# Kernel optimization log

Measured on AMD Instinct MI355X. Metric: run time of the kernel, lower is better.

## Reference

```python
import jax, jax.numpy as jnp
import numpy as np

D_MODEL = 512
NHEAD = 8
DIM = D_MODEL // NHEAD
EPS_ATT = 1e-6
EPS_LN = 1e-5


def layer_norm(x, gamma, beta):
    mu = jnp.mean(x, axis=-1, keepdims=True)
    var = jnp.mean(jnp.square(x - mu), axis=-1, keepdims=True)
    return (x - mu) * jax.lax.rsqrt(var + EPS_LN) * gamma + beta


def setup_inputs() -> dict:
    key = jax.random.key(0)
    ks = jax.random.split(key, 12)
    B, L = 4, 4096
    s = 1.0 / np.sqrt(D_MODEL)
    inp = {
        "q": jax.random.normal(ks[0], (B, L, D_MODEL), jnp.float32),
        "k": jax.random.normal(ks[1], (B, L, D_MODEL), jnp.float32),
        "v": jax.random.normal(ks[2], (B, L, D_MODEL), jnp.float32),
        # weights stored [in, out] so application is x @ W (== torch Linear with W.T)
        "Wq": jax.random.normal(ks[3], (D_MODEL, D_MODEL), jnp.float32) * s,
        "Wk": jax.random.normal(ks[4], (D_MODEL, D_MODEL), jnp.float32) * s,
        "Wv": jax.random.normal(ks[5], (D_MODEL, D_MODEL), jnp.float32) * s,
        "Wm": jax.random.normal(ks[6], (D_MODEL, D_MODEL), jnp.float32) * s,
        "W1": jax.random.normal(ks[7], (D_MODEL, 4 * D_MODEL), jnp.float32) * s,
        "W2": jax.random.normal(ks[8], (4 * D_MODEL, D_MODEL), jnp.float32) * (0.5 * s),
        "g1": jnp.ones((D_MODEL,), jnp.float32),
        "b1": jnp.zeros((D_MODEL,), jnp.float32),
        "g2": jnp.ones((D_MODEL,), jnp.float32),
        "b2": jnp.zeros((D_MODEL,), jnp.float32),
    }
    return inp


def reference(q, k, v, Wq, Wk, Wv, Wm, W1, W2, g1, b1, g2, b2):
    B, L, _ = q.shape
    S = k.shape[1]
    # projections -> [B, L, H, D]
    Qp = (q @ Wq).reshape(B, L, NHEAD, DIM)
    Kp = (k @ Wk).reshape(B, S, NHEAD, DIM)
    Vp = (v @ Wv).reshape(B, S, NHEAD, DIM)
    # elu+1 feature map linear attention
    Q = jax.nn.elu(Qp) + 1.0
    K = jax.nn.elu(Kp) + 1.0
    Vn = Vp / S
    KV = jnp.einsum('nshd,nshv->nhdv', K, Vn)          # [B,H,D,D]
    Z = 1.0 / (jnp.einsum('nlhd,nhd->nlh', Q, K.sum(axis=1)) + EPS_ATT)
    msg = jnp.einsum('nlhd,nhdv,nlh->nlhv', Q, KV, Z) * S  # [B,L,H,D]
    # merge + residual + norm1
    msg = msg.reshape(B, L, D_MODEL) @ Wm
    msg = layer_norm(msg + q, g1, b1)
    # FFN; note original adds mlp output to q (not norm1 output)
    ffn = jax.nn.relu(msg @ W1) @ W2
    out = layer_norm(q + ffn, g2, b2)
    return out
```

## Files before the change

kernel.cpp:

```cpp
#include <hip/hip_runtime.h>

typedef unsigned short u16;
typedef unsigned int u32;

typedef __bf16 bf16x8 __attribute__((ext_vector_type(8)));
typedef float f32x4 __attribute__((ext_vector_type(4)));

#define EPI_BF16 0
#define EPI_ELU1 1
#define EPI_RELU 2
#define EPI_ADDRES_F32 3

__device__ __forceinline__ float bf2f(u16 x) {
    u32 u = ((u32)x) << 16;
    return __uint_as_float(u);
}
__device__ __forceinline__ u16 f2bf(float f) {
    u32 u = __float_as_uint(f);
    u32 r = (u + 0x7FFFu + ((u >> 16) & 1u)) >> 16;
    return (u16)r;
}

__device__ __forceinline__ void gload_lds16(const u16* g, u16* l) {
    __builtin_amdgcn_global_load_lds(
        (const __attribute__((address_space(1))) u32*)g,
        (__attribute__((address_space(3))) u32*)l, 16, 0, 0);
}

__global__ __launch_bounds__(256) void f2b_k(const float* __restrict__ in,
                                             u16* __restrict__ out, int n) {
    int i = (blockIdx.x * 256 + threadIdx.x) * 4;
    if (i >= n) return;
    float4 f = *(const float4*)(in + i);
    ushort4 o;
    o.x = f2bf(f.x); o.y = f2bf(f.y); o.z = f2bf(f.z); o.w = f2bf(f.w);
    *(ushort4*)(out + i) = o;
}

__global__ void transpose_k(const float* __restrict__ in, u16* __restrict__ out,
                            int R, int C) {
    int idx = blockIdx.x * 256 + threadIdx.x;
    if (idx >= R * C) return;
    int c = idx / R, r = idx % R;
    out[idx] = f2bf(in[(long)r * C + c]);
}

__global__ __launch_bounds__(256) void gemm_bt(
    const u16* __restrict__ A, const u16* __restrict__ Bt,
    void* __restrict__ C, const float* __restrict__ Res,
    int M, int N, int K, int epi)
{
    __shared__ __align__(16) u16 As[2][128 * 32];
    __shared__ __align__(16) u16 Bs[2][128 * 32];

    int t = threadIdx.x;

    int gx = gridDim.x;
    int nwg = gx * gridDim.y;
    int bid = blockIdx.y * gx + blockIdx.x;
    if ((nwg & 7) == 0) {
        int cpx = nwg >> 3;
        bid = (bid & 7) * cpx + (bid >> 3);
    }
    int m0 = (bid / gx) * 128, n0 = (bid % gx) * 128;

    int wave = t >> 6, lane = t & 63;
    int wm = (wave >> 1) * 64, wn = (wave & 1) * 64;
    int lrow = lane & 15, lk8 = (lane >> 4) * 8;

    f32x4 acc[4][4] = {};

    int srow = wave * 16 + (lane >> 2);
    int scol = (lane & 3) * 8;
    const u16* pA0 = A + (long)(m0 + srow) * K + scol;
    const u16* pB0 = Bt + (long)(n0 + srow) * K + scol;
    const long s64 = (long)64 * K;

    int nt = K >> 5;
    int cur = 0;

    {
        u16* a = As[0] + wave * 512;
        u16* b = Bs[0] + wave * 512;
        gload_lds16(pA0, a);
        gload_lds16(pA0 + s64, a + 2048);
        gload_lds16(pB0, b);
        gload_lds16(pB0 + s64, b + 2048);
    }
    __builtin_amdgcn_s_waitcnt(0);
    __syncthreads();

    for (int kt = 0; kt < nt; ++kt) {
        if (kt + 1 < nt) {
            int k0 = (kt + 1) << 5;
            u16* a = As[cur ^ 1] + wave * 512;
            u16* b = Bs[cur ^ 1] + wave * 512;
            gload_lds16(pA0 + k0, a);
            gload_lds16(pA0 + s64 + k0, a + 2048);
            gload_lds16(pB0 + k0, b);
            gload_lds16(pB0 + s64 + k0, b + 2048);
        }

        const u16* As_c = As[cur];
        const u16* Bs_c = Bs[cur];
        bf16x8 af[4], bfr[4];
#pragma unroll
        for (int mi = 0; mi < 4; mi++)
            af[mi] = *(const bf16x8*)(As_c + (wm + mi * 16 + lrow) * 32 + lk8);
#pragma unroll
        for (int ni = 0; ni < 4; ni++)
            bfr[ni] = *(const bf16x8*)(Bs_c + (wn + ni * 16 + lrow) * 32 + lk8);
#pragma unroll
        for (int mi = 0; mi < 4; mi++)
#pragma unroll
            for (int ni = 0; ni < 4; ni++)
                acc[mi][ni] = __builtin_amdgcn_mfma_f32_16x16x32_bf16(
                    af[mi], bfr[ni], acc[mi][ni], 0, 0, 0);

        if (kt + 1 < nt) {
            __builtin_amdgcn_s_waitcnt(0);
            __syncthreads();
            cur ^= 1;
        }
    }

    int rq = (lane >> 4) * 4;
    int colb = n0 + wn + (lane & 15);
#pragma unroll
    for (int mi = 0; mi < 4; mi++) {
#pragma unroll
        for (int ni = 0; ni < 4; ni++) {
#pragma unroll
            for (int r = 0; r < 4; r++) {
                int row = m0 + wm + mi * 16 + rq + r;
                int col = colb + ni * 16;
                long idx = (long)row * N + col;
                float v0 = acc[mi][ni][r];
                if (epi == EPI_ELU1) {
                    float v = v0 > 0.f ? v0 + 1.f : __expf(v0);
                    ((u16*)C)[idx] = f2bf(v);
                } else if (epi == EPI_RELU) {
                    ((u16*)C)[idx] = f2bf(v0 > 0.f ? v0 : 0.f);
                } else if (epi == EPI_ADDRES_F32) {
                    ((float*)C)[idx] = v0 + Res[idx];
                } else {
                    ((u16*)C)[idx] = f2bf(v0);
                }
            }
        }
    }
}

__global__ __launch_bounds__(256) void kv_part(
    const u16* __restrict__ Kf, const u16* __restrict__ Vf,
    float* __restrict__ Part, float* __restrict__ KsPart)
{
    __shared__ float sKf[64 * 68];
    __shared__ float sVf[64 * 68];
    int bh = blockIdx.x;
    int b = bh >> 3, h = bh & 7;
    int s0 = blockIdx.y * 64;
    int t = threadIdx.x;
    int d = t & 63, vg = t >> 6;

    {
        int row = t >> 2, c16 = (t & 3) * 16;
        long g = ((long)b * 4096 + s0 + row) * 512 + h * 64 + c16;
        uint4 kk0 = *(const uint4*)(Kf + g);
        uint4 kk1 = *(const uint4*)(Kf + g + 8);
        uint4 vv0 = *(const uint4*)(Vf + g);
        uint4 vv1 = *(const uint4*)(Vf + g + 8);
        float* dk = sKf + row * 68 + c16;
        float* dv = sVf + row * 68 + c16;
        u32 kw[8] = {kk0.x, kk0.y, kk0.z, kk0.w, kk1.x, kk1.y, kk1.z, kk1.w};
        u32 vw[8] = {vv0.x, vv0.y, vv0.z, vv0.w, vv1.x, vv1.y, vv1.z, vv1.w};
#pragma unroll
        for (int j = 0; j < 8; j++) {
            dk[2 * j]     = __uint_as_float(kw[j] << 16);
            dk[2 * j + 1] = __uint_as_float(kw[j] & 0xFFFF0000u);
            dv[2 * j]     = __uint_as_float(vw[j] << 16);
            dv[2 * j + 1] = __uint_as_float(vw[j] & 0xFFFF0000u);
        }
    }
    __syncthreads();

    float acc[16] = {};
    float ks = 0.f;
#pragma unroll 4
    for (int s = 0; s < 64; s++) {
        float kd = sKf[s * 68 + d];
        if (vg == 0) ks += kd;
        const float* vr = sVf + s * 68 + vg * 16;
        float4 v0 = *(const float4*)(vr);
        float4 v1 = *(const float4*)(vr + 4);
        float4 v2 = *(const float4*)(vr + 8);
        float4 v3 = *(const float4*)(vr + 12);
        acc[0]  += kd * v0.x; acc[1]  += kd * v0.y;
        acc[2]  += kd * v0.z; acc[3]  += kd * v0.w;
        acc[4]  += kd * v1.x; acc[5]  += kd * v1.y;
        acc[6]  += kd * v1.z; acc[7]  += kd * v1.w;
        acc[8]  += kd * v2.x; acc[9]  += kd * v2.y;
        acc[10] += kd * v2.z; acc[11] += kd * v2.w;
        acc[12] += kd * v3.x; acc[13] += kd * v3.y;
        acc[14] += kd * v3.z; acc[15] += kd * v3.w;
    }
    float* pp = Part + ((long)bh * 64 + blockIdx.y) * 4096 + d * 64 + vg * 16;
#pragma unroll
    for (int j = 0; j < 16; j++) pp[j] = acc[j];
    if (vg == 0) KsPart[((bh * 64) + blockIdx.y) * 64 + d] = ks;
}

__global__ __launch_bounds__(256) void kv_reduce(
    const float* __restrict__ Part, const float* __restrict__ KsPart,
    float* __restrict__ KV, float* __restrict__ Ksum)
{
    int i = blockIdx.x * 256 + threadIdx.x;
    if (i < 131072) {
        int bh = i >> 12, dv = i & 4095;
        const float* p = Part + (long)bh * 64 * 4096 + dv;
        float s = 0.f;
#pragma unroll 8
        for (int sp = 0; sp < 64; sp++) s += p[(long)sp * 4096];
        KV[i] = s;
    } else if (i < 133120) {
        int j = i - 131072;
        int bh = j >> 6, d = j & 63;
        const float* p = KsPart + bh * 64 * 64 + d;
        float s = 0.f;
#pragma unroll 8
        for (int sp = 0; sp < 64; sp++) s += p[sp * 64];
        Ksum[j] = s;
    }
}

__global__ __launch_bounds__(256) void msg_k(
    const u16* __restrict__ Q, const float* __restrict__ KV,
    const float* __restrict__ Ksum, u16* __restrict__ Msg)
{
    __shared__ float sKVt[64 * 68];
    __shared__ float sQ[64 * 68];
    __shared__ float sKs[64];
    __shared__ float sZ[64];

    int bh = blockIdx.x;
    int b = bh >> 3, h = bh & 7;
    int l0 = blockIdx.y * 64;
    int t = threadIdx.x, wave = t >> 6, lane = t & 63;

    {
        const float* src = KV + (long)bh * 4096 + t * 16;
        int d = t >> 2;
        int v0 = (t & 3) * 16;
        float4 a0 = *(const float4*)(src);
        float4 a1 = *(const float4*)(src + 4);
        float4 a2 = *(const float4*)(src + 8);
        float4 a3 = *(const float4*)(src + 12);
        float tmp[16] = {a0.x, a0.y, a0.z, a0.w, a1.x, a1.y, a1.z, a1.w,
                         a2.x, a2.y, a2.z, a2.w, a3.x, a3.y, a3.z, a3.w};
#pragma unroll
        for (int j = 0; j < 16; j++) sKVt[(v0 + j) * 68 + d] = tmp[j];
    }
    {
        int row = t >> 2, c = (t & 3) * 16;
        const u16* src = Q + ((long)b * 4096 + l0 + row) * 512 + h * 64 + c;
        uint4 q0 = *(const uint4*)(src);
        uint4 q1 = *(const uint4*)(src + 8);
        float* dq = sQ + row * 68 + c;
        u32 qw[8] = {q0.x, q0.y, q0.z, q0.w, q1.x, q1.y, q1.z, q1.w};
#pragma unroll
        for (int j = 0; j < 8; j++) {
            dq[2 * j]     = __uint_as_float(qw[j] << 16);
            dq[2 * j + 1] = __uint_as_float(qw[j] & 0xFFFF0000u);
        }
    }
    if (t < 64) sKs[t] = Ksum[bh * 64 + t];
    __syncthreads();

    float kv[64];
    {
        const float* kr = sKVt + lane * 68;
#pragma unroll
        for (int j = 0; j < 16; j++) {
            float4 x = *(const float4*)(kr + 4 * j);
            kv[4 * j]     = x.x; kv[4 * j + 1] = x.y;
            kv[4 * j + 2] = x.z; kv[4 * j + 3] = x.w;
        }
    }
    if (t < 64) {
        const float* qr = sQ + t * 68;
        float zp = 0.f;
#pragma unroll
        for (int d = 0; d < 64; d++) zp += qr[d] * sKs[d];
        sZ[t] = 1.f / (zp + 1e-6f);
    }
    __syncthreads();

    const long obase = ((long)b * 4096 + l0) * 512 + h * 64 + lane;
    int lbase = wave * 16;
#pragma unroll 4
    for (int i = 0; i < 16; i++) {
        int ll = lbase + i;
        const float* qr = sQ + ll * 68;
        float a0 = 0.f, a1 = 0.f, a2 = 0.f, a3 = 0.f;
#pragma unroll
        for (int db = 0; db < 16; db++) {
            float4 q4 = *(const float4*)(qr + 4 * db);
            a0 += q4.x * kv[4 * db];
            a1 += q4.y * kv[4 * db + 1];
            a2 += q4.z * kv[4 * db + 2];
            a3 += q4.w * kv[4 * db + 3];
        }
        float acc = (a0 + a1) + (a2 + a3);
        Msg[obase + (long)ll * 512] = f2bf(acc * sZ[ll]);
    }
}

__global__ __launch_bounds__(256) void ln_k(
    const float* __restrict__ X, const float* __restrict__ g,
    const float* __restrict__ bta, u16* __restrict__ OutB,
    float* __restrict__ OutF, int out_f32)
{
    int row = blockIdx.x;
    const float* x = X + (long)row * 512;
    int t = threadIdx.x;
    float x0 = x[t], x1 = x[t + 256];
    float s = x0 + x1, sq = x0 * x0 + x1 * x1;
#pragma unroll
    for (int off = 32; off > 0; off >>= 1) {
        s += __shfl_xor(s, off, 64);
        sq += __shfl_xor(sq, off, 64);
    }
    __shared__ float rs[4], rq[4];
    int wave = t >> 6, lane = t & 63;
    if (lane == 0) { rs[wave] = s; rq[wave] = sq; }
    __syncthreads();
    s = rs[0] + rs[1] + rs[2] + rs[3];
    sq = rq[0] + rq[1] + rq[2] + rq[3];
    float mu = s * (1.f / 512.f);
    float var = sq * (1.f / 512.f) - mu * mu;
    float rstd = rsqrtf(var + 1e-5f);
    float y0 = (x0 - mu) * rstd * g[t] + bta[t];
    float y1 = (x1 - mu) * rstd * g[t + 256] + bta[t + 256];
    if (out_f32) {
        OutF[(long)row * 512 + t] = y0;
        OutF[(long)row * 512 + t + 256] = y1;
    } else {
        OutB[(long)row * 512 + t] = f2bf(y0);
        OutB[(long)row * 512 + t + 256] = f2bf(y1);
    }
}

extern "C" void kernel_launch(void* const* d_in, const int* in_sizes, int n_in,
                              void* d_out, int out_size, void* d_ws, size_t ws_size,
                              hipStream_t stream) {
    const float* q  = (const float*)d_in[0];
    const float* k  = (const float*)d_in[1];
    const float* v  = (const float*)d_in[2];
    const float* Wq = (const float*)d_in[3];
    const float* Wk = (const float*)d_in[4];
    const float* Wv = (const float*)d_in[5];
    const float* Wm = (const float*)d_in[6];
    const float* W1 = (const float*)d_in[7];
    const float* W2 = (const float*)d_in[8];
    const float* g1 = (const float*)d_in[9];
    const float* b1 = (const float*)d_in[10];
    const float* g2 = (const float*)d_in[11];
    const float* b2 = (const float*)d_in[12];

    char* ws = (char*)d_ws;
    u16* WTq = (u16*)(ws + 0);
    u16* WTk = (u16*)(ws + 524288);
    u16* WTv = (u16*)(ws + 1048576);
    u16* WTm = (u16*)(ws + 1572864);
    u16* W1T = (u16*)(ws + 2097152);
    u16* W2T = (u16*)(ws + 4194304);
    u16* qc  = (u16*)(ws + 6291456);
    u16* kc  = (u16*)(ws + 23068672);
    u16* vc  = (u16*)(ws + 39845888);
    u16* Qb  = (u16*)(ws + 56623104);
    u16* Kb  = (u16*)(ws + 73400320);
    u16* Vb  = (u16*)(ws + 90177536);
    float* KVb = (float*)(ws + 106954752);
    float* KSb = (float*)(ws + 107479040);
    u16* Msg = (u16*)(ws + 107487232);
    float* Part = (float*)(ws + 23068672);
    float* KsPart = (float*)(ws + 6291456);
    float* xpre = (float*)(ws + 23068672);
    u16* x1  = qc;
    u16* Hid = (u16*)(ws + 56623104);

    f2b_k<<<dim3(8192), 256, 0, stream>>>(q, qc, 8388608);
    f2b_k<<<dim3(8192), 256, 0, stream>>>(k, kc, 8388608);
    f2b_k<<<dim3(8192), 256, 0, stream>>>(v, vc, 8388608);

    transpose_k<<<dim3(1024), 256, 0, stream>>>(Wq, WTq, 512, 512);
    transpose_k<<<dim3(1024), 256, 0, stream>>>(Wk, WTk, 512, 512);
    transpose_k<<<dim3(1024), 256, 0, stream>>>(Wv, WTv, 512, 512);
    transpose_k<<<dim3(1024), 256, 0, stream>>>(Wm, WTm, 512, 512);
    transpose_k<<<dim3(4096), 256, 0, stream>>>(W1, W1T, 512, 2048);
    transpose_k<<<dim3(4096), 256, 0, stream>>>(W2, W2T, 2048, 512);

    gemm_bt<<<dim3(4, 128), 256, 0, stream>>>(qc, WTq, Qb, nullptr, 16384, 512, 512, EPI_ELU1);
    gemm_bt<<<dim3(4, 128), 256, 0, stream>>>(kc, WTk, Kb, nullptr, 16384, 512, 512, EPI_ELU1);
    gemm_bt<<<dim3(4, 128), 256, 0, stream>>>(vc, WTv, Vb, nullptr, 16384, 512, 512, EPI_BF16);

    kv_part<<<dim3(32, 64), 256, 0, stream>>>(Kb, Vb, Part, KsPart);
    kv_reduce<<<dim3(520), 256, 0, stream>>>(Part, KsPart, KVb, KSb);
    msg_k<<<dim3(32, 64), 256, 0, stream>>>(Qb, KVb, KSb, Msg);

    gemm_bt<<<dim3(4, 128), 256, 0, stream>>>(Msg, WTm, xpre, q, 16384, 512, 512, EPI_ADDRES_F32);
    ln_k<<<dim3(16384), 256, 0, stream>>>(xpre, g1, b1, x1, nullptr, 0);

    gemm_bt<<<dim3(16, 128), 256, 0, stream>>>(x1, W1T, Hid, nullptr, 16384, 2048, 512, EPI_RELU);
    gemm_bt<<<dim3(4, 128), 256, 0, stream>>>(Hid, W2T, xpre, q, 16384, 512, 2048, EPI_ADDRES_F32);
    ln_k<<<dim3(16384), 256, 0, stream>>>(xpre, g2, b2, nullptr, (float*)d_out, 1);
}
```

Measured before the change: 519.9 us.

## Deepen GEMM LDS pipeline to four stages with k-group-major LDS layout

Replaces the double-buffered LDS pipeline in the bf16 GEMM with a 4-buffer ring that prefetches three k-tiles ahead. It uses partial vmcnt waits so outstanding global->LDS loads can overlap compute instead of draining every iteration. It also changes the staging layout so each lane loads one row's 8-element k-group and LDS is stored k-group-major, making MFMA fragment reads contiguous and likely reducing bank conflicts. LDS usage doubles to 64KB per block, which may reduce occupancy. Correctness now depends on the hand-counted vmcnt values.

```diff
diff --git a/kernel.cpp b/kernel.cpp
--- a/kernel.cpp
+++ b/kernel.cpp
@@ -50,8 +50,8 @@
     void* __restrict__ C, const float* __restrict__ Res,
     int M, int N, int K, int epi)
 {
-    __shared__ __align__(16) u16 As[2][128 * 32];
-    __shared__ __align__(16) u16 Bs[2][128 * 32];
+    __shared__ __align__(16) u16 As[4][4096];
+    __shared__ __align__(16) u16 Bs[4][4096];
 
     int t = threadIdx.x;
 
@@ -66,62 +66,61 @@
 
     int wave = t >> 6, lane = t & 63;
     int wm = (wave >> 1) * 64, wn = (wave & 1) * 64;
-    int lrow = lane & 15, lk8 = (lane >> 4) * 8;
+    int lrow = lane & 15;
+    int lg = lane >> 4;
 
     f32x4 acc[4][4] = {};
 
-    int srow = wave * 16 + (lane >> 2);
-    int scol = (lane & 3) * 8;
-    const u16* pA0 = A + (long)(m0 + srow) * K + scol;
-    const u16* pB0 = Bt + (long)(n0 + srow) * K + scol;
-    const long s64 = (long)64 * K;
+    int srow = (wave & 1) * 64 + lane;
+    int sg8 = (wave >> 1) * 8;
+    const u16* pA0 = A + (long)(m0 + srow) * K + sg8;
+    const u16* pB0 = Bt + (long)(n0 + srow) * K + sg8;
 
     int nt = K >> 5;
-    int cur = 0;
-
-    {
-        u16* a = As[0] + wave * 512;
-        u16* b = Bs[0] + wave * 512;
-        gload_lds16(pA0, a);
-        gload_lds16(pA0 + s64, a + 2048);
-        gload_lds16(pB0, b);
-        gload_lds16(pB0 + s64, b + 2048);
-    }
-    __builtin_amdgcn_s_waitcnt(0);
-    __syncthreads();
+
+    for (int pt = 0; pt < 3 && pt < nt; ++pt) {
+        int k0 = pt << 5;
+        u16* a = As[pt] + wave * 512;
+        u16* b = Bs[pt] + wave * 512;
+        gload_lds16(pA0 + k0, a);
+        gload_lds16(pA0 + k0 + 16, a + 2048);
+        gload_lds16(pB0 + k0, b);
+        gload_lds16(pB0 + k0 + 16, b + 2048);
+    }
 
     for (int kt = 0; kt < nt; ++kt) {
-        if (kt + 1 < nt) {
-            int k0 = (kt + 1) << 5;
-            u16* a = As[cur ^ 1] + wave * 512;
-            u16* b = Bs[cur ^ 1] + wave * 512;
+        int rem = nt - 1 - kt;
+        if (rem >= 2)      asm volatile("s_waitcnt vmcnt(8)" ::: "memory");
+        else if (rem == 1) asm volatile("s_waitcnt vmcnt(4)" ::: "memory");
+        else               asm volatile("s_waitcnt vmcnt(0)" ::: "memory");
+        __builtin_amdgcn_s_barrier();
+        __builtin_amdgcn_sched_barrier(0);
+
+        if (kt + 3 < nt) {
+            int k0 = (kt + 3) << 5;
+            u16* a = As[(kt + 3) & 3] + wave * 512;
+            u16* b = Bs[(kt + 3) & 3] + wave * 512;
             gload_lds16(pA0 + k0, a);
-            gload_lds16(pA0 + s64 + k0, a + 2048);
+            gload_lds16(pA0 + k0 + 16, a + 2048);
             gload_lds16(pB0 + k0, b);
-            gload_lds16(pB0 + s64 + k0, b + 2048);
-        }
-
-        const u16* As_c = As[cur];
-        const u16* Bs_c = Bs[cur];
+            gload_lds16(pB0 + k0 + 16, b + 2048);
+        }
+
+        const u16* As_c = As[kt & 3] + lg * 1024;
+        const u16* Bs_c = Bs[kt & 3] + lg * 1024;
         bf16x8 af[4], bfr[4];
 #pragma unroll
         for (int mi = 0; mi < 4; mi++)
-            af[mi] = *(const bf16x8*)(As_c + (wm + mi * 16 + lrow) * 32 + lk8);
+            af[mi] = *(const bf16x8*)(As_c + (wm + mi * 16 + lrow) * 8);
 #pragma unroll
         for (int ni = 0; ni < 4; ni++)
-            bfr[ni] = *(const bf16x8*)(Bs_c + (wn + ni * 16 + lrow) * 32 + lk8);
+            bfr[ni] = *(const bf16x8*)(Bs_c + (wn + ni * 16 + lrow) * 8);
 #pragma unroll
         for (int mi = 0; mi < 4; mi++)
 #pragma unroll
             for (int ni = 0; ni < 4; ni++)
                 acc[mi][ni] = __builtin_amdgcn_mfma_f32_16x16x32_bf16(
                     af[mi], bfr[ni], acc[mi][ni], 0, 0, 0);
-
-        if (kt + 1 < nt) {
-            __builtin_amdgcn_s_waitcnt(0);
-            __syncthreads();
-            cur ^= 1;
-        }
     }
 
     int rq = (lane >> 4) * 4;
```

New measurement: 599.4 us. 15.3% more time.

## Merge QKV projections into one GEMM, remap LDS tile layout, halve kv_part splits

Applied to the files above, without the earlier changes.

The three Q/K/V projection GEMMs become a single 12x128-block launch. Each block picks its input and output third from its column offset and applies the ELU+1 or identity epilogue to match. The GEMM staging layout changes so each lane loads a 64-row stripe with k-groups stored in separate 1024-element LDS planes, which changes LDS read addressing, likely to reduce bank conflicts. kv_part now processes two 64-row chunks per block, halving the partial buffers and the kv_reduce loop length. The merged launch relies on qc/kc/vc, WTq/WTk/WTv and Qb/Kb/Vb sitting contiguously in the workspace with those exact strides.

```diff
diff --git a/kernel.cpp b/kernel.cpp
--- a/kernel.cpp
+++ b/kernel.cpp
@@ -10,6 +10,7 @@
 #define EPI_ELU1 1
 #define EPI_RELU 2
 #define EPI_ADDRES_F32 3
+#define EPI_PROJ3 4
 
 __device__ __forceinline__ float bf2f(u16 x) {
     u32 u = ((u32)x) << 16;
@@ -50,8 +51,8 @@
     void* __restrict__ C, const float* __restrict__ Res,
     int M, int N, int K, int epi)
 {
-    __shared__ __align__(16) u16 As[2][128 * 32];
-    __shared__ __align__(16) u16 Bs[2][128 * 32];
+    __shared__ __align__(16) u16 As[2][4096];
+    __shared__ __align__(16) u16 Bs[2][4096];
 
     int t = threadIdx.x;
 
@@ -64,17 +65,23 @@
     }
     int m0 = (bid / gx) * 128, n0 = (bid % gx) * 128;
 
+    int third = 0;
+    if (epi == EPI_PROJ3) {
+        third = n0 >> 9;
+        A += (long)third * 8388608;
+    }
+
     int wave = t >> 6, lane = t & 63;
     int wm = (wave >> 1) * 64, wn = (wave & 1) * 64;
-    int lrow = lane & 15, lk8 = (lane >> 4) * 8;
+    int lrow = lane & 15;
+    int lg = lane >> 4;
 
     f32x4 acc[4][4] = {};
 
-    int srow = wave * 16 + (lane >> 2);
-    int scol = (lane & 3) * 8;
-    const u16* pA0 = A + (long)(m0 + srow) * K + scol;
-    const u16* pB0 = Bt + (long)(n0 + srow) * K + scol;
-    const long s64 = (long)64 * K;
+    int srow = (wave & 1) * 64 + lane;
+    int sg8 = (wave >> 1) * 8;
+    const u16* pA0 = A + (long)(m0 + srow) * K + sg8;
+    const u16* pB0 = Bt + (long)(n0 + srow) * K + sg8;
 
     int nt = K >> 5;
     int cur = 0;
@@ -83,9 +90,9 @@
         u16* a = As[0] + wave * 512;
         u16* b = Bs[0] + wave * 512;
         gload_lds16(pA0, a);
-        gload_lds16(pA0 + s64, a + 2048);
+        gload_lds16(pA0 + 16, a + 2048);
         gload_lds16(pB0, b);
-        gload_lds16(pB0 + s64, b + 2048);
+        gload_lds16(pB0 + 16, b + 2048);
     }
     __builtin_amdgcn_s_waitcnt(0);
     __syncthreads();
@@ -96,20 +103,20 @@
             u16* a = As[cur ^ 1] + wave * 512;
             u16* b = Bs[cur ^ 1] + wave * 512;
             gload_lds16(pA0 + k0, a);
-            gload_lds16(pA0 + s64 + k0, a + 2048);
+            gload_lds16(pA0 + k0 + 16, a + 2048);
             gload_lds16(pB0 + k0, b);
-            gload_lds16(pB0 + s64 + k0, b + 2048);
-        }
-
-        const u16* As_c = As[cur];
-        const u16* Bs_c = Bs[cur];
+            gload_lds16(pB0 + k0 + 16, b + 2048);
+        }
+
+        const u16* As_c = As[cur] + lg * 1024;
+        const u16* Bs_c = Bs[cur] + lg * 1024;
         bf16x8 af[4], bfr[4];
 #pragma unroll
         for (int mi = 0; mi < 4; mi++)
-            af[mi] = *(const bf16x8*)(As_c + (wm + mi * 16 + lrow) * 32 + lk8);
+            af[mi] = *(const bf16x8*)(As_c + (wm + mi * 16 + lrow) * 8);
 #pragma unroll
         for (int ni = 0; ni < 4; ni++)
-            bfr[ni] = *(const bf16x8*)(Bs_c + (wn + ni * 16 + lrow) * 32 + lk8);
+            bfr[ni] = *(const bf16x8*)(Bs_c + (wn + ni * 16 + lrow) * 8);
 #pragma unroll
         for (int mi = 0; mi < 4; mi++)
 #pragma unroll
@@ -134,17 +141,26 @@
             for (int r = 0; r < 4; r++) {
                 int row = m0 + wm + mi * 16 + rq + r;
                 int col = colb + ni * 16;
-                long idx = (long)row * N + col;
                 float v0 = acc[mi][ni][r];
-                if (epi == EPI_ELU1) {
-                    float v = v0 > 0.f ? v0 + 1.f : __expf(v0);
-                    ((u16*)C)[idx] = f2bf(v);
-                } else if (epi == EPI_RELU) {
-                    ((u16*)C)[idx] = f2bf(v0 > 0.f ? v0 : 0.f);
-                } else if (epi == EPI_ADDRES_F32) {
-                    ((float*)C)[idx] = v0 + Res[idx];
+                if (epi == EPI_PROJ3) {
+                    u16* Cb = (u16*)C + (long)third * 8388608;
+                    long idx = (long)row * 512 + (col - (third << 9));
+                    float v = (third < 2)
+                                  ? (v0 > 0.f ? v0 + 1.f : __expf(v0))
+                                  : v0;
+                    Cb[idx] = f2bf(v);
                 } else {
-                    ((u16*)C)[idx] = f2bf(v0);
+                    long idx = (long)row * N + col;
+                    if (epi == EPI_ELU1) {
+                        float v = v0 > 0.f ? v0 + 1.f : __expf(v0);
+                        ((u16*)C)[idx] = f2bf(v);
+                    } else if (epi == EPI_RELU) {
+                        ((u16*)C)[idx] = f2bf(v0 > 0.f ? v0 : 0.f);
+                    } else if (epi == EPI_ADDRES_F32) {
+                        ((float*)C)[idx] = v0 + Res[idx];
+                    } else {
+                        ((u16*)C)[idx] = f2bf(v0);
+                    }
                 }
             }
         }
@@ -159,55 +175,60 @@
     __shared__ float sVf[64 * 68];
     int bh = blockIdx.x;
     int b = bh >> 3, h = bh & 7;
-    int s0 = blockIdx.y * 64;
     int t = threadIdx.x;
     int d = t & 63, vg = t >> 6;
 
-    {
-        int row = t >> 2, c16 = (t & 3) * 16;
-        long g = ((long)b * 4096 + s0 + row) * 512 + h * 64 + c16;
-        uint4 kk0 = *(const uint4*)(Kf + g);
-        uint4 kk1 = *(const uint4*)(Kf + g + 8);
-        uint4 vv0 = *(const uint4*)(Vf + g);
-        uint4 vv1 = *(const uint4*)(Vf + g + 8);
-        float* dk = sKf + row * 68 + c16;
-        float* dv = sVf + row * 68 + c16;
-        u32 kw[8] = {kk0.x, kk0.y, kk0.z, kk0.w, kk1.x, kk1.y, kk1.z, kk1.w};
-        u32 vw[8] = {vv0.x, vv0.y, vv0.z, vv0.w, vv1.x, vv1.y, vv1.z, vv1.w};
-#pragma unroll
-        for (int j = 0; j < 8; j++) {
-            dk[2 * j]     = __uint_as_float(kw[j] << 16);
-            dk[2 * j + 1] = __uint_as_float(kw[j] & 0xFFFF0000u);
-            dv[2 * j]     = __uint_as_float(vw[j] << 16);
-            dv[2 * j + 1] = __uint_as_float(vw[j] & 0xFFFF0000u);
-        }
-    }
-    __syncthreads();
-
     float acc[16] = {};
     float ks = 0.f;
+
+    for (int st = 0; st < 2; ++st) {
+        int s0 = blockIdx.y * 128 + st * 64;
+        {
+            int row = t >> 2, c16 = (t & 3) * 16;
+            long g = ((long)b * 4096 + s0 + row) * 512 + h * 64 + c16;
+            uint4 kk0 = *(const uint4*)(Kf + g);
+            uint4 kk1 = *(const uint4*)(Kf + g + 8);
+            uint4 vv0 = *(const uint4*)(Vf + g);
+            uint4 vv1 = *(const uint4*)(Vf + g + 8);
+            float* dk = sKf + row * 68 + c16;
+            float* dv = sVf + row * 68 + c16;
+            u32 kw[8] = {kk0.x, kk0.y, kk0.z, kk0.w, kk1.x, kk1.y, kk1.z, kk1.w};
+            u32 vw[8] = {vv0.x, vv0.y, vv0.z, vv0.w, vv1.x, vv1.y, vv1.z, vv1.w};
+#pragma unroll
+            for (int j = 0; j < 8; j++) {
+                dk[2 * j]     = __uint_as_float(kw[j] << 16);
+                dk[2 * j + 1] = __uint_as_float(kw[j] & 0xFFFF0000u);
+                dv[2 * j]     = __uint_as_float(vw[j] << 16);
+                dv[2 * j + 1] = __uint_as_float(vw[j] & 0xFFFF0000u);
+            }
+        }
+        __syncthreads();
+
 #pragma unroll 4
-    for (int s = 0; s < 64; s++) {
-        float kd = sKf[s * 68 + d];
-        if (vg == 0) ks += kd;
-        const float* vr = sVf + s * 68 + vg * 16;
-        float4 v0 = *(const float4*)(vr);
-        float4 v1 = *(const float4*)(vr + 4);
-        float4 v2 = *(const float4*)(vr + 8);
-        float4 v3 = *(const float4*)(vr + 12);
-        acc[0]  += kd * v0.x; acc[1]  += kd * v0.y;
-        acc[2]  += kd * v0.z; acc[3]  += kd * v0.w;
-        acc[4]  += kd * v1.x; acc[5]  += kd * v1.y;
-        acc[6]  += kd * v1.z; acc[7]  += kd * v1.w;
-        acc[8]  += kd * v2.x; acc[9]  += kd * v2.y;
-        acc[10] += kd * v2.z; acc[11] += kd * v2.w;
-        acc[12] += kd * v3.x; acc[13] += kd * v3.y;
-        acc[14] += kd * v3.z; acc[15] += kd * v3.w;
-    }
-    float* pp = Part + ((long)bh * 64 + blockIdx.y) * 4096 + d * 64 + vg * 16;
+        for (int s = 0; s < 64; s++) {
+            float kd = sKf[s * 68 + d];
+            if (vg == 0) ks += kd;
+            const float* vr = sVf + s * 68 + vg * 16;
+            float4 v0 = *(const float4*)(vr);
+            float4 v1 = *(const float4*)(vr + 4);
+            float4 v2 = *(const float4*)(vr + 8);
+            float4 v3 = *(const float4*)(vr + 12);
+            acc[0]  += kd * v0.x; acc[1]  += kd * v0.y;
+            acc[2]  += kd * v0.z; acc[3]  += kd * v0.w;
+            acc[4]  += kd * v1.x; acc[5]  += kd * v1.y;
+            acc[6]  += kd * v1.z; acc[7]  += kd * v1.w;
+            acc[8]  += kd * v2.x; acc[9]  += kd * v2.y;
+            acc[10] += kd * v2.z; acc[11] += kd * v2.w;
+            acc[12] += kd * v3.x; acc[13] += kd * v3.y;
+            acc[14] += kd * v3.z; acc[15] += kd * v3.w;
+        }
+        __syncthreads();
+    }
+
+    float* pp = Part + ((long)bh * 32 + blockIdx.y) * 4096 + d * 64 + vg * 16;
 #pragma unroll
     for (int j = 0; j < 16; j++) pp[j] = acc[j];
-    if (vg == 0) KsPart[((bh * 64) + blockIdx.y) * 64 + d] = ks;
+    if (vg == 0) KsPart[((bh * 32) + blockIdx.y) * 64 + d] = ks;
 }
 
 __global__ __launch_bounds__(256) void kv_reduce(
@@ -217,18 +238,18 @@
     int i = blockIdx.x * 256 + threadIdx.x;
     if (i < 131072) {
         int bh = i >> 12, dv = i & 4095;
-        const float* p = Part + (long)bh * 64 * 4096 + dv;
+        const float* p = Part + (long)bh * 32 * 4096 + dv;
         float s = 0.f;
 #pragma unroll 8
-        for (int sp = 0; sp < 64; sp++) s += p[(long)sp * 4096];
+        for (int sp = 0; sp < 32; sp++) s += p[(long)sp * 4096];
         KV[i] = s;
     } else if (i < 133120) {
         int j = i - 131072;
         int bh = j >> 6, d = j & 63;
-        const float* p = KsPart + bh * 64 * 64 + d;
+        const float* p = KsPart + bh * 32 * 64 + d;
         float s = 0.f;
 #pragma unroll 8
-        for (int sp = 0; sp < 64; sp++) s += p[sp * 64];
+        for (int sp = 0; sp < 32; sp++) s += p[sp * 64];
         Ksum[j] = s;
     }
 }
@@ -400,11 +421,9 @@
     transpose_k<<<dim3(4096), 256, 0, stream>>>(W1, W1T, 512, 2048);
     transpose_k<<<dim3(4096), 256, 0, stream>>>(W2, W2T, 2048, 512);
 
-    gemm_bt<<<dim3(4, 128), 256, 0, stream>>>(qc, WTq, Qb, nullptr, 16384, 512, 512, EPI_ELU1);
-    gemm_bt<<<dim3(4, 128), 256, 0, stream>>>(kc, WTk, Kb, nullptr, 16384, 512, 512, EPI_ELU1);
-    gemm_bt<<<dim3(4, 128), 256, 0, stream>>>(vc, WTv, Vb, nullptr, 16384, 512, 512, EPI_BF16);
-
-    kv_part<<<dim3(32, 64), 256, 0, stream>>>(Kb, Vb, Part, KsPart);
+    gemm_bt<<<dim3(12, 128), 256, 0, stream>>>(qc, WTq, Qb, nullptr, 16384, 1536, 512, EPI_PROJ3);
+
+    kv_part<<<dim3(32, 32), 256, 0, stream>>>(Kb, Vb, Part, KsPart);
     kv_reduce<<<dim3(520), 256, 0, stream>>>(Part, KsPart, KVb, KSb);
     msg_k<<<dim3(32, 64), 256, 0, stream>>>(Qb, KVb, KSb, Msg);
 
```

New measurement: 570.8 us. +9.8%, slower.
